# Performance work log

Hardware: AMD Instinct MI355X
Metric: run time of the kernel (lower is better)

Reference implementation:

```python
import jax, jax.numpy as jnp
import numpy as np

B, S, E, H = 2, 2048, 2048, 16
D = E // H

def setup_inputs() -> dict:
    key = jax.random.key(0)
    ks = jax.random.split(key, 9)
    sc = 1.0 / np.sqrt(E)
    return {
        "x":  jax.random.normal(ks[0], (B, S, E), jnp.float32),
        "Wq": jax.random.normal(ks[1], (E, E), jnp.float32) * sc,
        "bq": jax.random.normal(ks[2], (E,), jnp.float32) * 0.01,
        "Wk": jax.random.normal(ks[3], (E, E), jnp.float32) * sc,
        "bk": jax.random.normal(ks[4], (E,), jnp.float32) * 0.01,
        "Wv": jax.random.normal(ks[5], (E, E), jnp.float32) * sc,
        "bv": jax.random.normal(ks[6], (E,), jnp.float32) * 0.01,
        "Wo": jax.random.normal(ks[7], (E, E), jnp.float32) * sc,
        "bo": jax.random.normal(ks[8], (E,), jnp.float32) * 0.01,
    }

def _split_heads(t):
    # [B,S,E] -> [B,H,S,D]
    return t.reshape(B, S, H, D).transpose(0, 2, 1, 3)

def reference(x, Wq, bq, Wk, bk, Wv, bv, Wo, bo):
    # projections (nn.Linear: y = x @ W^T + b)
    q = _split_heads(x @ Wq.T + bq)
    k = _split_heads(x @ Wk.T + bk)
    v = _split_heads(x @ Wv.T + bv)

    # scaled causal attention; scale uses k.size(-1) == head_dim D
    scores = jnp.einsum("bhqd,bhkd->bhqk", q, k) / jnp.sqrt(jnp.asarray(D, q.dtype))
    causal = jnp.tril(jnp.ones((S, S), bool))  # [S,S]
    scores = jnp.where(causal[None, None, :, :], scores, -jnp.inf)
    # training path subtracts row max before softmax (no-op under stable softmax)
    scores = scores - jnp.max(scores, axis=-1, keepdims=True)
    attn = jax.nn.softmax(scores, axis=-1)
    # dropout_rate = 0.0 -> identity
    ctx = jnp.einsum("bhqk,bhkd->bhqd", attn, v)

    # merge heads [B,H,S,D] -> [B,S,E], final projection
    out = ctx.transpose(0, 2, 1, 3).reshape(B, S, E)
    return out @ Wo.T + bo
```

## Files before the change

kernel.cpp:

```cpp
#include <hip/hip_runtime.h>

typedef unsigned short u16;
typedef __attribute__((ext_vector_type(4))) float f32x4;
typedef __attribute__((ext_vector_type(8))) short s16x8;
typedef __attribute__((ext_vector_type(4))) unsigned short u16x4;

#define MFMA16(a, b, c) __builtin_amdgcn_mfma_f32_16x16x32_bf16((a), (b), (c), 0, 0, 0)

__device__ __forceinline__ u16 f2bf(float f) {
  union { float f; unsigned u; } v; v.f = f;
  unsigned u = v.u;
  u += 0x7fffu + ((u >> 16) & 1u);
  return (u16)(u >> 16);
}

__device__ __forceinline__ void gl_lds16(const void* g, void* l) {
  __builtin_amdgcn_global_load_lds(
      (const __attribute__((address_space(1))) void*)g,
      (__attribute__((address_space(3))) void*)l, 16, 0, 0);
}

__global__ void cast6(const float* __restrict__ x,
                      const float* __restrict__ w0, const float* __restrict__ w1,
                      const float* __restrict__ w2, const float* __restrict__ w3,
                      u16* __restrict__ ws) {
  const int y = blockIdx.y;
  const float* src;
  u16* dst;
  if (y < 2) { src = x + (size_t)y * 4194304; dst = ws + (size_t)y * 4194304; }
  else {
    src = (y == 2) ? w0 : (y == 3) ? w1 : (y == 4) ? w2 : w3;
    dst = ws + 8388608 + (size_t)(y - 2) * 4194304;
  }
  const int i = blockIdx.x * 256 + threadIdx.x;
  f32x4 v = ((const f32x4*)src)[i];
  u16x4 o;
#pragma unroll
  for (int e = 0; e < 4; ++e) o[e] = f2bf(v[e]);
  ((u16x4*)dst)[i] = o;
}

template <int SWAP>
__device__ __forceinline__ void gemm_core(const u16* __restrict__ A,
                                          const u16* __restrict__ Bw,
                                          u16* sA, u16* sB,
                                          f32x4 (&acc)[4][4],
                                          int m0, int n0, int tid) {
  const int lane = tid & 63, w = tid >> 6;
  const int ln = lane & 15, quad = lane >> 4, ln7 = ln & 7;
  const int wm = (w >> 1) * 64, wn = (w & 1) * 64;
  const int srow = lane >> 3;
  const int scol = (((lane & 7) ^ srow)) * 8;

  for (int k0 = 0; k0 < 2048; k0 += 64) {
#pragma unroll
    for (int c = 0; c < 4; ++c) {
      const int chunk = c * 4 + w;
      const int row = chunk * 8 + srow;
      gl_lds16(A + (size_t)(m0 + row) * 2048 + k0 + scol, (char*)sA + chunk * 1024);
      gl_lds16(Bw + (size_t)(n0 + row) * 2048 + k0 + scol, (char*)sB + chunk * 1024);
    }
    __syncthreads();
#pragma unroll
    for (int kk = 0; kk < 64; kk += 32) {
      s16x8 af[4], bf[4];
      const int g = (kk >> 3) + quad;
#pragma unroll
      for (int t = 0; t < 4; ++t) {
        af[t] = *(const s16x8*)&sA[(wm + t * 16 + ln) * 64 + ((g ^ ln7) << 3)];
        bf[t] = *(const s16x8*)&sB[(wn + t * 16 + ln) * 64 + ((g ^ ln7) << 3)];
      }
#pragma unroll
      for (int tm = 0; tm < 4; ++tm)
#pragma unroll
        for (int tn = 0; tn < 4; ++tn)
          acc[tm][tn] = SWAP ? MFMA16(bf[tn], af[tm], acc[tm][tn])
                             : MFMA16(af[tm], bf[tn], acc[tm][tn]);
    }
    __syncthreads();
  }
}

__global__ __launch_bounds__(512, 2) void gemm_qk256(
    const u16* __restrict__ A,
    const u16* __restrict__ W0, const u16* __restrict__ W1,
    const float* __restrict__ b0, const float* __restrict__ b1,
    u16* __restrict__ Qo, u16* __restrict__ Ko) {
  __shared__ __align__(16) u16 smem[65536];
  const int z = blockIdx.z;
  const u16* Bw = z ? W1 : W0;
  const float* bias = z ? b1 : b0;
  u16* out = z ? Ko : Qo;
  const float scale = z ? 1.0f : 0.08838834764831845f;

  const int tid = threadIdx.x;
  const int lane = tid & 63, w = tid >> 6;
  const int ln = lane & 15, quad = lane >> 4, ln7 = lane & 7;
  const int m0 = blockIdx.y * 256, n0 = blockIdx.x * 256;
  const int wm = (w >> 2) << 7, wn = (w & 3) << 6;

  const int ci0 = tid, ci1 = 512 + tid;
  const int r0 = ci0 >> 3, c0k = ((ci0 & 7) ^ (r0 & 7)) << 3;
  const int r1 = ci1 >> 3, c1k = ((ci1 & 7) ^ (r1 & 7)) << 3;
  const int abase = (w >> 2) << 13;
  const int bbase = 16384 + (((w >> 1) & 1) << 13) + ((w & 1) << 12);
  const int sw0 = (quad ^ ln7) << 3, sw1 = ((4 + quad) ^ ln7) << 3;

  f32x4 acc[8][4] = {};
  s16x8 af[8][2], bf[4][2];

  auto STGA = [&](int t) {
    u16* dst = smem + ((t & 1) << 15);
    const int kc = (t & 31) << 6;
    const u16* s0 = A + (size_t)(m0 + r0) * 2048 + kc + c0k;
    const u16* s1 = A + (size_t)(m0 + r1) * 2048 + kc + c1k;
    gl_lds16(s0, dst + ci0 * 8);
    gl_lds16(s1, dst + ci1 * 8);
    gl_lds16(s0 + (size_t)128 * 2048, dst + 8192 + ci0 * 8);
    gl_lds16(s1 + (size_t)128 * 2048, dst + 8192 + ci1 * 8);
  };
  auto STGB = [&](int t) {
    u16* dst = smem + ((t & 1) << 15) + 16384;
    const int kc = (t & 31) << 6;
    const u16* s0 = Bw + (size_t)(n0 + r0) * 2048 + kc + c0k;
    const u16* s1 = Bw + (size_t)(n0 + r1) * 2048 + kc + c1k;
    gl_lds16(s0, dst + ci0 * 8);
    gl_lds16(s1, dst + ci1 * 8);
    gl_lds16(s0 + (size_t)128 * 2048, dst + 8192 + ci0 * 8);
    gl_lds16(s1 + (size_t)128 * 2048, dst + 8192 + ci1 * 8);
  };
  auto RDA = [&](int buf, int tm0) {
    const u16* p = smem + (buf << 15) + abase;
#pragma unroll
    for (int u = 0; u < 4; ++u) {
      const int tt = tm0 + u;
      af[tt][0] = *(const s16x8*)&p[(tt * 16 + ln) * 64 + sw0];
      af[tt][1] = *(const s16x8*)&p[(tt * 16 + ln) * 64 + sw1];
    }
  };
  auto RDB = [&](int buf, int tn0) {
    const u16* p = smem + (buf << 15) + bbase;
#pragma unroll
    for (int u = 0; u < 2; ++u) {
      const int tt = tn0 + u;
      bf[tt][0] = *(const s16x8*)&p[(tt * 16 + ln) * 64 + sw0];
      bf[tt][1] = *(const s16x8*)&p[(tt * 16 + ln) * 64 + sw1];
    }
  };
  auto QM = [&](int tm0, int tn0) {
    __builtin_amdgcn_s_setprio(1);
#pragma unroll
    for (int tm = tm0; tm < tm0 + 4; ++tm)
#pragma unroll
      for (int tn = tn0; tn < tn0 + 2; ++tn)
#pragma unroll
        for (int ks = 0; ks < 2; ++ks)
          acc[tm][tn] = MFMA16(bf[tn][ks], af[tm][ks], acc[tm][tn]);
    __builtin_amdgcn_s_setprio(0);
  };

#define BAR()                                   \
  asm volatile("" ::: "memory");                \
  __builtin_amdgcn_s_barrier();                 \
  asm volatile("" ::: "memory")
#define SEAL() asm volatile("s_waitcnt vmcnt(0)" ::: "memory")

  STGA(0); STGB(0); STGA(1);
  asm volatile("s_waitcnt vmcnt(4)" ::: "memory");
  BAR();
  RDA(0, 0); RDB(0, 0);

#pragma unroll 1
  for (int u = 0; u < 16; ++u) {
    const int t = 2 * u;
    QM(0, 0);
    RDA(0, 4);
    STGB(t + 1);
    BAR();
    QM(4, 0);
    RDB(0, 2);
    BAR();
    QM(4, 2);
    SEAL();
    BAR();
    QM(0, 2);
    RDA(1, 0); RDB(1, 0);
    STGA(t + 2);
    BAR();
    QM(0, 0);
    RDA(1, 4);
    STGB(t + 2);
    BAR();
    QM(4, 0);
    RDB(1, 2);
    BAR();
    QM(4, 2);
    SEAL();
    BAR();
    QM(0, 2);
    RDA(0, 0); RDB(0, 0);
    STGA(t + 3);
    BAR();
  }
  asm volatile("s_waitcnt vmcnt(0) lgkmcnt(0)" ::: "memory");
#undef BAR
#undef SEAL

#pragma unroll
  for (int tn = 0; tn < 4; ++tn) {
    const int n_base = n0 + wn + tn * 16 + quad * 4;
    const f32x4 bv = *(const f32x4*)&bias[n_base];
    const int h = n_base >> 7, dl = n_base & 127;
#pragma unroll
    for (int tm = 0; tm < 8; ++tm) {
      const int m = m0 + wm + tm * 16 + ln;
      const int b = m >> 11, s = m & 2047;
      u16x4 ov;
#pragma unroll
      for (int r = 0; r < 4; ++r) ov[r] = f2bf((acc[tm][tn][r] + bv[r]) * scale);
      *(u16x4*)&out[(((size_t)(b * 16 + h)) << 18) + ((size_t)s << 7) + dl] = ov;
    }
  }
}

__global__ __launch_bounds__(256, 2) void gemm_v(const u16* __restrict__ A,
                                                 const u16* __restrict__ Bw,
                                                 const float* __restrict__ bias,
                                                 u16* __restrict__ Vo) {
  __shared__ __align__(16) u16 smem[16384];
  u16* sA = smem;
  u16* sB = smem + 8192;
  const int tid = threadIdx.x;
  const int lane = tid & 63, w = tid >> 6;
  const int ln = lane & 15, quad = lane >> 4;
  const int m0 = blockIdx.y * 128, n0 = blockIdx.x * 128;
  const int wm = (w >> 1) * 64, wn = (w & 1) * 64;

  f32x4 acc[4][4] = {};
  gemm_core<0>(A, Bw, sA, sB, acc, m0, n0, tid);
  const int b = m0 >> 11;
#pragma unroll
  for (int tn = 0; tn < 4; ++tn) {
    const int n = n0 + wn + tn * 16 + ln;
    const float bv = bias[n];
    const int h = n >> 7, dl = n & 127;
#pragma unroll
    for (int tm = 0; tm < 4; ++tm) {
      const int s_base = (m0 & 2047) + wm + tm * 16 + quad * 4;
      u16x4 ov;
#pragma unroll
      for (int r = 0; r < 4; ++r) ov[r] = f2bf(acc[tm][tn][r] + bv);
      *(u16x4*)&Vo[(((size_t)((b * 16 + h) * 128 + dl)) << 11) + s_base] = ov;
    }
  }
}

__global__ __launch_bounds__(256, 2) void gemm_out(const u16* __restrict__ A,
                                                   const u16* __restrict__ Bw,
                                                   const float* __restrict__ bias,
                                                   float* __restrict__ out) {
  __shared__ __align__(16) u16 smem[16384];
  u16* sA = smem;
  u16* sB = smem + 8192;
  const int tid = threadIdx.x;
  const int lane = tid & 63, w = tid >> 6;
  const int ln = lane & 15, quad = lane >> 4;
  const int m0 = blockIdx.y * 128, n0 = blockIdx.x * 128;
  const int wm = (w >> 1) * 64, wn = (w & 1) * 64;

  f32x4 acc[4][4] = {};
  gemm_core<1>(A, Bw, sA, sB, acc, m0, n0, tid);
#pragma unroll
  for (int tn = 0; tn < 4; ++tn) {
    const int n_base = n0 + wn + tn * 16 + quad * 4;
    const f32x4 bv = *(const f32x4*)&bias[n_base];
#pragma unroll
    for (int tm = 0; tm < 4; ++tm) {
      const int m = m0 + wm + tm * 16 + ln;
      f32x4 ov;
#pragma unroll
      for (int r = 0; r < 4; ++r) ov[r] = acc[tm][tn][r] + bv[r];
      *(f32x4*)&out[(size_t)m * 2048 + n_base] = ov;
    }
  }
}

__global__ __launch_bounds__(256, 2) void attn_kernel(const u16* __restrict__ Q,
                                                      const u16* __restrict__ Kp,
                                                      const u16* __restrict__ Vt,
                                                      u16* __restrict__ ctx) {
  __shared__ __align__(16) u16 smem[24576];
  u16* sP = smem;
  u16* sK = smem + 8192;
  u16* sV = smem + 16384;

  const int flat = blockIdx.x + (blockIdx.y << 4);
  const int bh = flat >> 4;
  const int i = (flat < 256) ? (15 - (flat & 15)) : (flat & 15);
  const size_t base = (size_t)bh << 18;

  const int tid = threadIdx.x, lane = tid & 63, w = tid >> 6;
  const int ln = lane & 15, quad = lane >> 4, ln7 = lane & 7;

#pragma unroll
  for (int c = 0; c < 8; ++c) {
    const int chunk0 = (c * 4 + w) * 64;
    const int chunk = chunk0 + lane;
    const int row = chunk >> 4, cc = chunk & 15;
    gl_lds16(Q + base + (size_t)((i * 128 + row) * 128 + ((cc ^ (row & 15)) << 3)),
             (char*)sK + chunk0 * 16);
  }
  __syncthreads();
  s16x8 qf[2][4];
#pragma unroll
  for (int qt = 0; qt < 2; ++qt)
#pragma unroll
    for (int kc = 0; kc < 4; ++kc)
      qf[qt][kc] =
          *(const s16x8*)&sK[(w * 32 + qt * 16 + ln) * 128 + (((kc * 4 + quad) ^ ln) << 3)];
  __syncthreads();

  auto stageK = [&](int j) {
#pragma unroll
    for (int c = 0; c < 4; ++c) {
      const int chunk0 = (c * 4 + w) * 64;
      const int chunk = chunk0 + lane;
      const int row = chunk >> 4, cc = chunk & 15;
      gl_lds16(Kp + base + (size_t)((j * 64 + row) * 128 + ((cc ^ (row & 15)) << 3)),
               (char*)sK + chunk0 * 16);
    }
  };
  auto stageV = [&](int j) {
#pragma unroll
    for (int c = 0; c < 4; ++c) {
      const int chunk0 = (c * 4 + w) * 64;
      const int chunk = chunk0 + lane;
      const int row = chunk >> 3, cc = chunk & 7;
      gl_lds16(Vt + base + (size_t)(row * 2048 + j * 64 + ((cc ^ (row & 7)) << 3)),
               (char*)sV + chunk0 * 16);
    }
  };

  stageK(0);
  stageV(0);
  __syncthreads();

  f32x4 o_acc[8][2] = {};
  float lsum[2] = {0.f, 0.f};
  const int jmax = 2 * i + 1;
  const int qg = i * 128 + w * 32 + ln;

  for (int j = 0; j <= jmax; ++j) {
    f32x4 sacc[4][2] = {};
#pragma unroll
    for (int kc = 0; kc < 4; ++kc) {
      s16x8 kf[4];
#pragma unroll
      for (int kt = 0; kt < 4; ++kt)
        kf[kt] = *(const s16x8*)&sK[(kt * 16 + ln) * 128 + (((kc * 4 + quad) ^ ln) << 3)];
#pragma unroll
      for (int kt = 0; kt < 4; ++kt)
#pragma unroll
        for (int qt = 0; qt < 2; ++qt)
          sacc[kt][qt] = MFMA16(kf[kt], qf[qt][kc], sacc[kt][qt]);
    }

    const bool diag = (j >= 2 * i);
#pragma unroll
    for (int kt = 0; kt < 4; ++kt)
#pragma unroll
      for (int qt = 0; qt < 2; ++qt) {
        u16x4 pk;
#pragma unroll
        for (int r = 0; r < 4; ++r) {
          const int kg = j * 64 + kt * 16 + quad * 4 + r;
          float pv = __expf(sacc[kt][qt][r]);
          if (diag && kg > qg + qt * 16) pv = 0.f;
          lsum[qt] += pv;
          pk[r] = f2bf(pv);
        }
        const int qrow = w * 32 + qt * 16 + ln;
        const int c = kt * 4 + quad;
        *(u16x4*)&sP[qrow * 64 + ((c ^ (qrow & 14)) << 2)] = pk;
      }
    __syncthreads();
    if (j < jmax) stageK(j + 1);

#pragma unroll
    for (int kc = 0; kc < 2; ++kc) {
      s16x8 vf[8], pf[2];
#pragma unroll
      for (int qt = 0; qt < 2; ++qt) {
        const int qrow = w * 32 + qt * 16 + ln;
        const int c0 = kc * 8 + quad * 2;
        pf[qt] = *(const s16x8*)&sP[qrow * 64 + ((c0 ^ (qrow & 14)) << 2)];
      }
#pragma unroll
      for (int dt = 0; dt < 8; ++dt)
        vf[dt] = *(const s16x8*)&sV[(dt * 16 + ln) * 64 + (((kc * 4 + quad) ^ ln7) << 3)];
#pragma unroll
      for (int dt = 0; dt < 8; ++dt)
#pragma unroll
        for (int qt = 0; qt < 2; ++qt)
          o_acc[dt][qt] = MFMA16(vf[dt], pf[qt], o_acc[dt][qt]);
    }
    __syncthreads();
    if (j < jmax) stageV(j + 1);
  }

  const int b = bh >> 4, h = bh & 15;
  float rinv[2];
#pragma unroll
  for (int qt = 0; qt < 2; ++qt) {
    float s = lsum[qt];
    s += __shfl_xor(s, 16);
    s += __shfl_xor(s, 32);
    rinv[qt] = __builtin_amdgcn_rcpf(s);
  }
#pragma unroll
  for (int dt = 0; dt < 8; ++dt)
#pragma unroll
    for (int qt = 0; qt < 2; ++qt) {
      const int sg = i * 128 + w * 32 + qt * 16 + ln;
      const int d0 = h * 128 + dt * 16 + quad * 4;
      u16x4 ov;
#pragma unroll
      for (int r = 0; r < 4; ++r) ov[r] = f2bf(o_acc[dt][qt][r] * rinv[qt]);
      *(u16x4*)&ctx[((size_t)b << 22) + (size_t)sg * 2048 + d0] = ov;
    }
}

extern "C" void kernel_launch(void* const* d_in, const int* in_sizes, int n_in,
                              void* d_out, int out_size, void* d_ws, size_t ws_size,
                              hipStream_t stream) {
  const float* x = (const float*)d_in[0];
  const float* Wq = (const float*)d_in[1];
  const float* bq = (const float*)d_in[2];
  const float* Wk = (const float*)d_in[3];
  const float* bk = (const float*)d_in[4];
  const float* Wv = (const float*)d_in[5];
  const float* bv = (const float*)d_in[6];
  const float* Wo = (const float*)d_in[7];
  const float* bo = (const float*)d_in[8];

  u16* ws = (u16*)d_ws;
  u16* xb = ws;
  u16* Wqb = xb + 8388608;
  u16* Wkb = Wqb + 4194304;
  u16* Wvb = Wkb + 4194304;
  u16* Wob = Wvb + 4194304;
  u16* Qb = Wob + 4194304;
  u16* Kb = Qb + 8388608;
  u16* Vtb = Kb + 8388608;
  u16* ctxb = Vtb + 8388608;

  cast6<<<dim3(4096, 6), 256, 0, stream>>>(x, Wq, Wk, Wv, Wo, ws);

  gemm_qk256<<<dim3(8, 16, 2), 512, 0, stream>>>(xb, Wqb, Wkb, bq, bk, Qb, Kb);
  gemm_v<<<dim3(16, 32), 256, 0, stream>>>(xb, Wvb, bv, Vtb);

  attn_kernel<<<dim3(16, 32), 256, 0, stream>>>(Qb, Kb, Vtb, ctxb);

  gemm_out<<<dim3(16, 32), 256, 0, stream>>>(ctxb, Wob, bo, (float*)d_out);
}
```

Before: 356.2 us.

## Double-buffer K/V tiles in attention and use exp2 with packed bf16 converts

The attention kernel now double-buffers the K and V tiles in LDS. The next tile's loads are issued at the top of each iteration, so they overlap the current QK and PV math instead of being staged after barriers. The softmax scale has log2(e) folded into the Q projection so the kernel can call the hardware exp2, and probabilities are packed to bf16 with v_cvt_pk_bf16_f32. The barrier between the P write and the P read becomes a wave-local lgkmcnt wait, since each wave touches only its own P rows. LDS use grows to 80KB per block, which could limit occupancy at two blocks per CU.

After: 349.9 us. About the same (-1.8%).

```diff
diff --git a/kernel.cpp b/kernel.cpp
--- a/kernel.cpp
+++ b/kernel.cpp
@@ -4,6 +4,7 @@
 typedef __attribute__((ext_vector_type(4))) float f32x4;
 typedef __attribute__((ext_vector_type(8))) short s16x8;
 typedef __attribute__((ext_vector_type(4))) unsigned short u16x4;
+typedef __attribute__((ext_vector_type(2))) unsigned u32x2;
 
 #define MFMA16(a, b, c) __builtin_amdgcn_mfma_f32_16x16x32_bf16((a), (b), (c), 0, 0, 0)
 
@@ -12,6 +13,12 @@
   unsigned u = v.u;
   u += 0x7fffu + ((u >> 16) & 1u);
   return (u16)(u >> 16);
+}
+
+__device__ __forceinline__ unsigned cvtpk(float a, float b) {
+  unsigned r;
+  asm("v_cvt_pk_bf16_f32 %0, %1, %2" : "=v"(r) : "v"(a), "v"(b));
+  return r;
 }
 
 __device__ __forceinline__ void gl_lds16(const void* g, void* l) {
@@ -91,7 +98,7 @@
   const u16* Bw = z ? W1 : W0;
   const float* bias = z ? b1 : b0;
   u16* out = z ? Ko : Qo;
-  const float scale = z ? 1.0f : 0.08838834764831845f;
+  const float scale = z ? 1.0f : 0.1275174306003988f;
 
   const int tid = threadIdx.x;
   const int lane = tid & 63, w = tid >> 6;
@@ -289,10 +296,8 @@
                                                       const u16* __restrict__ Kp,
                                                       const u16* __restrict__ Vt,
                                                       u16* __restrict__ ctx) {
-  __shared__ __align__(16) u16 smem[24576];
+  __shared__ __align__(16) u16 smem[40960];
   u16* sP = smem;
-  u16* sK = smem + 8192;
-  u16* sV = smem + 16384;
 
   const int flat = blockIdx.x + (blockIdx.y << 4);
   const int bh = flat >> 4;
@@ -308,7 +313,7 @@
     const int chunk = chunk0 + lane;
     const int row = chunk >> 4, cc = chunk & 15;
     gl_lds16(Q + base + (size_t)((i * 128 + row) * 128 + ((cc ^ (row & 15)) << 3)),
-             (char*)sK + chunk0 * 16);
+             (char*)(smem + 8192) + chunk0 * 16);
   }
   __syncthreads();
   s16x8 qf[2][4];
@@ -316,33 +321,35 @@
   for (int qt = 0; qt < 2; ++qt)
 #pragma unroll
     for (int kc = 0; kc < 4; ++kc)
-      qf[qt][kc] =
-          *(const s16x8*)&sK[(w * 32 + qt * 16 + ln) * 128 + (((kc * 4 + quad) ^ ln) << 3)];
+      qf[qt][kc] = *(const s16x8*)&smem[8192 + (w * 32 + qt * 16 + ln) * 128 +
+                                        (((kc * 4 + quad) ^ ln) << 3)];
   __syncthreads();
 
-  auto stageK = [&](int j) {
+  auto stageK = [&](int j, int buf) {
+    u16* dst = smem + 8192 + buf * 8192;
 #pragma unroll
     for (int c = 0; c < 4; ++c) {
       const int chunk0 = (c * 4 + w) * 64;
       const int chunk = chunk0 + lane;
       const int row = chunk >> 4, cc = chunk & 15;
       gl_lds16(Kp + base + (size_t)((j * 64 + row) * 128 + ((cc ^ (row & 15)) << 3)),
-               (char*)sK + chunk0 * 16);
-    }
-  };
-  auto stageV = [&](int j) {
+               (char*)dst + chunk0 * 16);
+    }
+  };
+  auto stageV = [&](int j, int buf) {
+    u16* dst = smem + 24576 + buf * 8192;
 #pragma unroll
     for (int c = 0; c < 4; ++c) {
       const int chunk0 = (c * 4 + w) * 64;
       const int chunk = chunk0 + lane;
       const int row = chunk >> 3, cc = chunk & 7;
       gl_lds16(Vt + base + (size_t)(row * 2048 + j * 64 + ((cc ^ (row & 7)) << 3)),
-               (char*)sV + chunk0 * 16);
-    }
-  };
-
-  stageK(0);
-  stageV(0);
+               (char*)dst + chunk0 * 16);
+    }
+  };
+
+  stageK(0, 0);
+  stageV(0, 0);
   __syncthreads();
 
   f32x4 o_acc[8][2] = {};
@@ -351,6 +358,11 @@
   const int qg = i * 128 + w * 32 + ln;
 
   for (int j = 0; j <= jmax; ++j) {
+    const int cb = j & 1;
+    if (j < jmax) { stageK(j + 1, cb ^ 1); stageV(j + 1, cb ^ 1); }
+    const u16* sK = smem + 8192 + cb * 8192;
+    const u16* sV = smem + 24576 + cb * 8192;
+
     f32x4 sacc[4][2] = {};
 #pragma unroll
     for (int kc = 0; kc < 4; ++kc) {
@@ -370,21 +382,24 @@
     for (int kt = 0; kt < 4; ++kt)
 #pragma unroll
       for (int qt = 0; qt < 2; ++qt) {
-        u16x4 pk;
+        f32x4 pv;
 #pragma unroll
         for (int r = 0; r < 4; ++r) {
+          float p = __builtin_amdgcn_exp2f(sacc[kt][qt][r]);
           const int kg = j * 64 + kt * 16 + quad * 4 + r;
-          float pv = __expf(sacc[kt][qt][r]);
-          if (diag && kg > qg + qt * 16) pv = 0.f;
-          lsum[qt] += pv;
-          pk[r] = f2bf(pv);
+          if (diag && kg > qg + qt * 16) p = 0.f;
+          lsum[qt] += p;
+          pv[r] = p;
         }
+        u32x2 pk2;
+        pk2[0] = cvtpk(pv[0], pv[1]);
+        pk2[1] = cvtpk(pv[2], pv[3]);
         const int qrow = w * 32 + qt * 16 + ln;
         const int c = kt * 4 + quad;
-        *(u16x4*)&sP[qrow * 64 + ((c ^ (qrow & 14)) << 2)] = pk;
+        *(u32x2*)&sP[qrow * 64 + ((c ^ (qrow & 14)) << 2)] = pk2;
       }
-    __syncthreads();
-    if (j < jmax) stageK(j + 1);
+    asm volatile("s_waitcnt lgkmcnt(0)" ::: "memory");
+    __builtin_amdgcn_sched_barrier(0);
 
 #pragma unroll
     for (int kc = 0; kc < 2; ++kc) {
@@ -405,7 +420,6 @@
           o_acc[dt][qt] = MFMA16(vf[dt], pf[qt], o_acc[dt][qt]);
     }
     __syncthreads();
-    if (j < jmax) stageV(j + 1);
   }
 
   const int b = bh >> 4, h = bh & 15;
```
